# Kernel optimization log

Measured on AMD Instinct MI355X. Metric: run time of the kernel, lower is better.

Reference implementation:

```python
import jax, jax.numpy as jnp
import numpy as np

NEG_INF = -1.0e9  # masked_fill value in the original


def gaussian_prior(n_heads, len_q, len_k, dtype=jnp.float32):
    """Per-head lower-triangular Gaussian positional bias.

    gm[h, i, j] = exp(-(j - i)^2 / (2 * sigma_h^2)) for i >= j, else 0.
    The buggy source never passes sigma_hs; we use sigma_h = h + 1 as a
    deterministic per-head bandwidth (wider Gaussians for later heads).
    """
    i = jnp.arange(len_q)[:, None]          # [Lq, 1]
    j = jnp.arange(len_k)[None, :]          # [1, Lk]
    d2 = (j - i).astype(dtype) ** 2         # [Lq, Lk]
    sigma = jnp.arange(1, n_heads + 1, dtype=dtype)  # [H]
    g = jnp.exp(-d2[None] / (2.0 * sigma[:, None, None] ** 2))  # [H, Lq, Lk]
    return jnp.where(i >= j, g, jnp.zeros((), dtype))[None]     # mask upper tri -> [1,H,Lq,Lk] via broadcast of where


def setup_inputs() -> dict:
    key = jax.random.key(0)
    kq, kk, kv = jax.random.split(key, 3)
    B, H, S, D = 2, 16, 2048, 128
    Q = jax.random.normal(kq, (B, H, S, D), dtype=jnp.float32)
    K = jax.random.normal(kk, (B, H, S, D), dtype=jnp.float32)
    V = jax.random.normal(kv, (B, H, S, D), dtype=jnp.float32)
    # Causal mask: True where attention is disallowed (j > i), broadcastable.
    i = jnp.arange(S)[:, None]
    j = jnp.arange(S)[None, :]
    attn_mask = (j > i)[None, None]  # [1,1,S,S] bool
    return {"Q": Q, "K": K, "V": V, "attn_mask": attn_mask}


def reference(Q, K, V, attn_mask):
    B, H, Lq, D = Q.shape
    Lk = K.shape[2]
    scale = 1.0 / np.sqrt(D).astype(np.float32)
    # scores: [B,H,Lq,Lk]
    scores = jnp.einsum("bhqd,bhkd->bhqk", Q, K) * scale
    gm = gaussian_prior(H, Lq, Lk, dtype=scores.dtype)  # [H,Lq,Lk] broadcast over batch
    scores = scores + gm
    scores = jnp.where(attn_mask, jnp.asarray(NEG_INF, scores.dtype), scores)
    attn = jax.nn.softmax(scores, axis=-1)
    context = jnp.einsum("bhqk,bhkd->bhqd", attn, V)
    return (context, attn)
```

## Files before the change

### kernel.cpp

```cpp
#include <hip/hip_runtime.h>

typedef __attribute__((ext_vector_type(8))) short s16x8;
typedef __attribute__((ext_vector_type(4))) float f32x4;


static __device__ __forceinline__ unsigned short f2bf(float f) {
  unsigned int u = __float_as_uint(f);
  u += 0x7fffu + ((u >> 16) & 1u);
  return (unsigned short)(u >> 16);
}

static __device__ __forceinline__ unsigned short* swz(unsigned short* base, int row,
                                                      int shift, int byte_in_row) {
  int b = (row << shift) + (byte_in_row ^ ((row & 7) << 4));
  return (unsigned short*)((char*)base + b);
}

static __device__ __forceinline__ s16x8 pack8(float4 a, float4 b) {
  s16x8 p;
  p[0] = (short)f2bf(a.x); p[1] = (short)f2bf(a.y);
  p[2] = (short)f2bf(a.z); p[3] = (short)f2bf(a.w);
  p[4] = (short)f2bf(b.x); p[5] = (short)f2bf(b.y);
  p[6] = (short)f2bf(b.z); p[7] = (short)f2bf(b.w);
  return p;
}

#define GLDS(gp, lp) __builtin_amdgcn_global_load_lds(                        \
    (const __attribute__((address_space(1))) void*)(gp),                      \
    (__attribute__((address_space(3))) void*)(lp), 16, 0, 0)

#define STAGE(ldsbase, gtile) do {                                            \
    const char* _g = (const char*)(gtile) + (w << 12) + (lane << 4);          \
    char* _l = (char*)(ldsbase) + (w << 12);                                  \
    GLDS(_g,        _l);                                                      \
    GLDS(_g + 1024, _l + 1024);                                               \
    GLDS(_g + 2048, _l + 2048);                                               \
    GLDS(_g + 3072, _l + 3072);                                               \
  } while (0)

#define C_L2E   1.4426950408889634f
#define C_SCL2  (0.08838834764831845f * C_L2E)
#define C_B1    (-11.541560327111707f)


__global__ void pack_kv(const float* __restrict__ Kg, const float* __restrict__ Vg,
                        unsigned short* __restrict__ Kw, unsigned short* __restrict__ Vw) {
  __shared__ float Vs[8192];
  const int blk = (int)blockIdx.x;
  const float* Kb = Kg + ((size_t)blk << 13);
  const float* Vb = Vg + ((size_t)blk << 13);
  unsigned short* Ko = Kw + ((size_t)blk << 13);
  unsigned short* Vo = Vw + ((size_t)blk << 13);
  int c = (int)threadIdx.x;
  #pragma unroll
  for (int it = 0; it < 4; ++it, c += 256) {
    int r = c >> 4, c8 = (c & 15) << 3;
    int dst = r * 128 + ((((c8 << 1)) ^ ((r & 7) << 4)) >> 1);
    const float4* s4 = (const float4*)(Kb + r * 128 + c8);
    *(s16x8*)(Ko + dst) = pack8(s4[0], s4[1]);
  }
  c = (int)threadIdx.x;
  #pragma unroll
  for (int it = 0; it < 8; ++it, c += 256)
    *(float4*)(Vs + (c << 2)) = *(const float4*)(Vb + (c << 2));
  __syncthreads();
  c = (int)threadIdx.x;
  #pragma unroll
  for (int it = 0; it < 4; ++it, c += 256) {
    int d = c & 127, j0 = (c >> 7) << 3;
    s16x8 p;
    #pragma unroll
    for (int e = 0; e < 8; ++e) p[e] = (short)f2bf(Vs[(j0 + e) * 128 + d]);
    int dst = d * 64 + ((((j0 << 1)) ^ ((d & 7) << 4)) >> 1);
    *(s16x8*)(Vo + dst) = p;
  }
}


__global__ __launch_bounds__(256, 2)
void gpsdpa9(const float* __restrict__ Qg, const unsigned short* __restrict__ Kw,
             const unsigned short* __restrict__ Vw, float* __restrict__ Og,
             float* __restrict__ Ag) {
  __shared__ alignas(16) unsigned short KV[32768];
  __shared__ alignas(16) unsigned short Ps[4][1024];

  const int tid  = (int)threadIdx.x;
  const int w    = tid >> 6;
  const int lane = tid & 63;
  const int l15  = lane & 15;
  const int g    = lane >> 4;

  const int bh = (int)blockIdx.x & 31;
  const int qt = 31 - ((int)blockIdx.x >> 5);
  const int h  = bh & 15;
  const int q0 = qt << 6;

  const float* Qb = Qg + ((size_t)bh << 18) + ((size_t)q0 << 7);
  const unsigned short* Kb = Kw + ((size_t)(bh << 5) << 13);
  const unsigned short* Vb = Vw + ((size_t)(bh << 5) << 13);
  float* Ob = Og + ((size_t)bh << 18) + ((size_t)q0 << 7);
  float* Ab = Ag + ((size_t)bh << 22);

  const float cst2 = (-1.0f / (2.0f * (float)(h + 1) * (float)(h + 1))) * C_L2E;

  s16x8 aQ[4];
  {
    const float* qr = Qb + ((w << 4) + l15) * 128 + (g << 3);
    #pragma unroll
    for (int kc = 0; kc < 4; ++kc) {
      const float4* s4 = (const float4*)(qr + (kc << 5));
      aQ[kc] = pack8(s4[0], s4[1]);
    }
  }

  const int ibase = q0 + (w << 4) + (g << 2);
  const f32x4 fzero = {0.f, 0.f, 0.f, 0.f};

  float ps_acc[4] = {0.f, 0.f, 0.f, 0.f};

  const int nst = (qt >> 1) + 1;
  STAGE(&KV[0],    Kb);
  STAGE(&KV[8192], Kb + ((size_t)1 << 13));
  for (int s = 0; s < nst; ++s) {
    const int cur = s & 1;
    __syncthreads();
    if (s + 1 < nst) {
      unsigned short* nb = &KV[(cur ^ 1) << 14];
      STAGE(nb,        Kb + ((size_t)(2 * s + 2) << 13));
      STAGE(nb + 8192, Kb + ((size_t)(2 * s + 3) << 13));
    }
    #pragma unroll
    for (int half = 0; half < 2; ++half) {
      const int t = 2 * s + half;
      if (t > qt) break;
      unsigned short* Kt = &KV[(cur << 14) + (half << 13)];

      f32x4 acc[4];
      #pragma unroll
      for (int n = 0; n < 4; ++n) acc[n] = fzero;
      __builtin_amdgcn_s_setprio(1);
      #pragma unroll
      for (int kc = 0; kc < 4; ++kc) {
        #pragma unroll
        for (int n = 0; n < 4; ++n) {
          s16x8 bK = *(const s16x8*)swz(Kt, (n << 4) + l15, 8, (kc << 6) + (g << 4));
          acc[n] = __builtin_amdgcn_mfma_f32_16x16x32_bf16(aQ[kc], bK, acc[n], 0, 0, 0);
        }
      }
      __builtin_amdgcn_s_setprio(0);

      const int jb = (t << 6) + l15;
      if (t <= qt - 3) {
        #pragma unroll
        for (int r = 0; r < 4; ++r) {
          float sm = 0.f;
          #pragma unroll
          for (int n = 0; n < 4; ++n)
            sm += __builtin_amdgcn_exp2f(fmaf(acc[n][r], C_SCL2, C_B1));
          ps_acc[r] += sm;
        }
      } else if (t < qt) {
        #pragma unroll
        for (int r = 0; r < 4; ++r) {
          const int i = ibase + r;
          float sm = 0.f;
          #pragma unroll
          for (int n = 0; n < 4; ++n) {
            float fd = (float)(i - (jb + (n << 4)));
            float gl = __builtin_amdgcn_exp2f(fd * fd * cst2);
            sm += __builtin_amdgcn_exp2f(fmaf(acc[n][r], C_SCL2, fmaf(gl, C_L2E, C_B1)));
          }
          ps_acc[r] += sm;
        }
      } else {
        #pragma unroll
        for (int r = 0; r < 4; ++r) {
          const int i = ibase + r;
          float sm = 0.f;
          #pragma unroll
          for (int n = 0; n < 4; ++n) {
            int dist = i - (jb + (n << 4));
            float fd = (float)dist;
            float gl = __builtin_amdgcn_exp2f(fd * fd * cst2);
            float x = __builtin_amdgcn_exp2f(fmaf(acc[n][r], C_SCL2, fmaf(gl, C_L2E, C_B1)));
            sm += (dist >= 0) ? x : 0.f;
          }
          ps_acc[r] += sm;
        }
      }
    }
  }

  float lrs2[4];
  #pragma unroll
  for (int r = 0; r < 4; ++r) {
    float v = ps_acc[r];
    #pragma unroll
    for (int mk = 1; mk < 16; mk <<= 1) v += __shfl_xor(v, mk, 64);
    lrs2[r] = C_B1 - __log2f(v);
  }

  f32x4 oacc[8];
  #pragma unroll
  for (int dn = 0; dn < 8; ++dn) oacc[dn] = fzero;

  unsigned short* Pw = &Ps[w][0];

  __syncthreads();
  STAGE(&KV[0],     Kb);
  STAGE(&KV[16384], Vb);

  for (int t = 0; t <= qt; ++t) {
    const int cur = t & 1;
    __syncthreads();
    if (t < qt) {
      STAGE(&KV[(cur ^ 1) << 13],           Kb + ((size_t)(t + 1) << 13));
      STAGE(&KV[16384 + ((cur ^ 1) << 13)], Vb + ((size_t)(t + 1) << 13));
    }
    unsigned short* Kt = &KV[cur << 13];
    unsigned short* Vt = &KV[16384 + (cur << 13)];

    f32x4 acc[4];
    #pragma unroll
    for (int n = 0; n < 4; ++n) acc[n] = fzero;
    __builtin_amdgcn_s_setprio(1);
    #pragma unroll
    for (int kc = 0; kc < 4; ++kc) {
      #pragma unroll
      for (int n = 0; n < 4; ++n) {
        s16x8 bK = *(const s16x8*)swz(Kt, (n << 4) + l15, 8, (kc << 6) + (g << 4));
        acc[n] = __builtin_amdgcn_mfma_f32_16x16x32_bf16(aQ[kc], bK, acc[n], 0, 0, 0);
      }
    }
    __builtin_amdgcn_s_setprio(0);

    const int jb = (t << 6) + l15;
    if (t <= qt - 3) {
      #pragma unroll
      for (int r = 0; r < 4; ++r) {
        const int i = ibase + r;
        #pragma unroll
        for (int n = 0; n < 4; ++n) {
          float p = __builtin_amdgcn_exp2f(fmaf(acc[n][r], C_SCL2, lrs2[r]));
          Ab[(size_t)i * 2048 + jb + (n << 4)] = p;
          *swz(Pw, (g << 2) + r, 7, ((n << 4) + l15) << 1) = f2bf(p);
        }
      }
    } else if (t < qt) {
      #pragma unroll
      for (int r = 0; r < 4; ++r) {
        const int i = ibase + r;
        #pragma unroll
        for (int n = 0; n < 4; ++n) {
          float fd = (float)(i - (jb + (n << 4)));
          float gl = __builtin_amdgcn_exp2f(fd * fd * cst2);
          float p = __builtin_amdgcn_exp2f(fmaf(acc[n][r], C_SCL2, fmaf(gl, C_L2E, lrs2[r])));
          Ab[(size_t)i * 2048 + jb + (n << 4)] = p;
          *swz(Pw, (g << 2) + r, 7, ((n << 4) + l15) << 1) = f2bf(p);
        }
      }
    } else {
      #pragma unroll
      for (int r = 0; r < 4; ++r) {
        const int i = ibase + r;
        #pragma unroll
        for (int n = 0; n < 4; ++n) {
          int dist = i - (jb + (n << 4));
          float fd = (float)dist;
          float gl = __builtin_amdgcn_exp2f(fd * fd * cst2);
          float x = __builtin_amdgcn_exp2f(fmaf(acc[n][r], C_SCL2, fmaf(gl, C_L2E, lrs2[r])));
          float p = (dist >= 0) ? x : 0.f;
          Ab[(size_t)i * 2048 + jb + (n << 4)] = p;
          *swz(Pw, (g << 2) + r, 7, ((n << 4) + l15) << 1) = f2bf(p);
        }
      }
    }

    __builtin_amdgcn_s_setprio(1);
    #pragma unroll
    for (int kc2 = 0; kc2 < 2; ++kc2) {
      s16x8 pa = *(const s16x8*)swz(Pw, l15, 7, (kc2 << 6) + (g << 4));
      #pragma unroll
      for (int dn = 0; dn < 8; ++dn) {
        s16x8 vb = *(const s16x8*)swz(Vt, (dn << 4) + l15, 7, (kc2 << 6) + (g << 4));
        oacc[dn] = __builtin_amdgcn_mfma_f32_16x16x32_bf16(pa, vb, oacc[dn], 0, 0, 0);
      }
    }
    __builtin_amdgcn_s_setprio(0);
  }

  #pragma unroll
  for (int dn = 0; dn < 8; ++dn) {
    #pragma unroll
    for (int r = 0; r < 4; ++r) {
      Ob[(size_t)((w << 4) + (g << 2) + r) * 128 + (dn << 4) + l15] = oacc[dn][r];
    }
  }

  const float4 z4 = make_float4(0.f, 0.f, 0.f, 0.f);
  for (int tt = qt + 1; tt < 32; ++tt) {
    float4* dst = (float4*)(Ab + (size_t)q0 * 2048 + (tt << 6));
    int f = tid;
    #pragma unroll
    for (int k = 0; k < 4; ++k, f += 256) {
      int r = f >> 4, cc = f & 15;
      dst[(size_t)r * 512 + cc] = z4;
    }
  }
}


__global__ __launch_bounds__(256, 2)
void gpsdpa_fb(const float* __restrict__ Qg, const float* __restrict__ Kg,
               const float* __restrict__ Vg, float* __restrict__ Og,
               float* __restrict__ Ag) {
  __shared__ alignas(16) unsigned short Qs[64 * 128];
  __shared__ alignas(16) unsigned short Ksl[64 * 128];
  __shared__ alignas(16) unsigned short Vtl[128 * 64];
  __shared__ alignas(16) unsigned short Ps[4][16 * 64];
  __shared__ float gtab[2048];

  const int tid  = (int)threadIdx.x;
  const int w    = tid >> 6;
  const int lane = tid & 63;
  const int l15  = lane & 15;
  const int g    = lane >> 4;

  const int bh = (int)blockIdx.x & 31;
  const int qt = 31 - ((int)blockIdx.x >> 5);
  const int h  = bh & 15;
  const int q0 = qt << 6;

  const size_t base = (size_t)bh << 18;
  const float* Qb = Qg + base + (size_t)q0 * 128;
  const float* Kb = Kg + base;
  const float* Vb = Vg + base;
  float* Ob = Og + base;
  float* Ab = Ag + ((size_t)bh << 22);

  {
    float sig = (float)(h + 1);
    float c = -1.0f / (2.0f * sig * sig);
    for (int d = tid; d < 2048; d += 256) {
      float fd = (float)d;
      gtab[d] = __expf(fd * fd * c);
    }
  }

  {
    int c = tid;
    #pragma unroll
    for (int it = 0; it < 4; ++it, c += 256) {
      int r = c >> 4, c8 = (c & 15) << 3;
      const float4* s4 = (const float4*)(Qb + (size_t)r * 128 + c8);
      *(s16x8*)swz(Qs, r, 8, c8 * 2) = pack8(s4[0], s4[1]);
    }
  }
  __syncthreads();

  s16x8 aQ[4];
  #pragma unroll
  for (int kc = 0; kc < 4; ++kc)
    aQ[kc] = *(const s16x8*)swz(Qs, (w << 4) + l15, 8, (kc << 6) + (g << 4));

  const float scale = 0.08838834764831845f;
  const int ibase = q0 + (w << 4) + (g << 2);

  float m_r[4], ls_r[4];
  #pragma unroll
  for (int r = 0; r < 4; ++r) { m_r[r] = -3.0e38f; ls_r[r] = 0.0f; }

  const f32x4 fzero = {0.f, 0.f, 0.f, 0.f};

  for (int t = 0; t <= qt; ++t) {
    __syncthreads();
    {
      int c = tid;
      #pragma unroll
      for (int it = 0; it < 4; ++it, c += 256) {
        int r = c >> 4, c8 = (c & 15) << 3;
        const float4* s4 = (const float4*)(Kb + (size_t)((t << 6) + r) * 128 + c8);
        *(s16x8*)swz(Ksl, r, 8, c8 * 2) = pack8(s4[0], s4[1]);
      }
    }
    __syncthreads();

    f32x4 acc[4];
    #pragma unroll
    for (int n = 0; n < 4; ++n) acc[n] = fzero;
    #pragma unroll
    for (int kc = 0; kc < 4; ++kc) {
      #pragma unroll
      for (int n = 0; n < 4; ++n) {
        s16x8 bK = *(const s16x8*)swz(Ksl, (n << 4) + l15, 8, (kc << 6) + (g << 4));
        acc[n] = __builtin_amdgcn_mfma_f32_16x16x32_bf16(aQ[kc], bK, acc[n], 0, 0, 0);
      }
    }

    const int jb = (t << 6) + l15;
    #pragma unroll
    for (int r = 0; r < 4; ++r) {
      const int i = ibase + r;
      float sv[4];
      float mx = -3.0e38f;
      #pragma unroll
      for (int n = 0; n < 4; ++n) {
        int dist = i - (jb + (n << 4));
        float x = (dist >= 0) ? (acc[n][r] * scale + gtab[dist]) : -1.0e9f;
        sv[n] = x;
        mx = fmaxf(mx, x);
      }
      #pragma unroll
      for (int mk = 1; mk < 16; mk <<= 1) mx = fmaxf(mx, __shfl_xor(mx, mk, 64));
      float mn = fmaxf(m_r[r], mx);
      float sm = 0.f;
      #pragma unroll
      for (int n = 0; n < 4; ++n) sm += __expf(sv[n] - mn);
      #pragma unroll
      for (int mk = 1; mk < 16; mk <<= 1) sm += __shfl_xor(sm, mk, 64);
      ls_r[r] = ls_r[r] * __expf(m_r[r] - mn) + sm;
      m_r[r] = mn;
    }
  }

  float rls[4];
  #pragma unroll
  for (int r = 0; r < 4; ++r) rls[r] = 1.0f / ls_r[r];

  f32x4 oacc[8];
  #pragma unroll
  for (int dn = 0; dn < 8; ++dn) oacc[dn] = fzero;

  unsigned short* Pw = &Ps[w][0];

  for (int t = 0; t <= qt; ++t) {
    __syncthreads();
    {
      int c = tid;
      #pragma unroll
      for (int it = 0; it < 4; ++it, c += 256) {
        int r = c >> 4, c8 = (c & 15) << 3;
        const float4* s4 = (const float4*)(Kb + (size_t)((t << 6) + r) * 128 + c8);
        *(s16x8*)swz(Ksl, r, 8, c8 * 2) = pack8(s4[0], s4[1]);
      }
      c = tid;
      #pragma unroll
      for (int it = 0; it < 4; ++it, c += 256) {
        int d = c & 127, j0 = (c >> 7) << 3;
        const float* vs = Vb + (size_t)((t << 6) + j0) * 128 + d;
        s16x8 p;
        #pragma unroll
        for (int e = 0; e < 8; ++e) p[e] = (short)f2bf(vs[(size_t)e * 128]);
        *(s16x8*)swz(Vtl, d, 7, j0 * 2) = p;
      }
    }
    __syncthreads();

    f32x4 acc[4];
    #pragma unroll
    for (int n = 0; n < 4; ++n) acc[n] = fzero;
    #pragma unroll
    for (int kc = 0; kc < 4; ++kc) {
      #pragma unroll
      for (int n = 0; n < 4; ++n) {
        s16x8 bK = *(const s16x8*)swz(Ksl, (n << 4) + l15, 8, (kc << 6) + (g << 4));
        acc[n] = __builtin_amdgcn_mfma_f32_16x16x32_bf16(aQ[kc], bK, acc[n], 0, 0, 0);
      }
    }

    const int jb = (t << 6) + l15;
    #pragma unroll
    for (int r = 0; r < 4; ++r) {
      const int i = ibase + r;
      float* arow = Ab + (size_t)i * 2048 + (t << 6) + l15;
      #pragma unroll
      for (int n = 0; n < 4; ++n) {
        int dist = i - (jb + (n << 4));
        float x = (dist >= 0) ? (acc[n][r] * scale + gtab[dist]) : -1.0e9f;
        float p = __expf(x - m_r[r]) * rls[r];
        arow[n << 4] = p;
        *swz(Pw, (g << 2) + r, 7, ((n << 4) + l15) << 1) = f2bf(p);
      }
    }

    #pragma unroll
    for (int kc2 = 0; kc2 < 2; ++kc2) {
      s16x8 pa = *(const s16x8*)swz(Pw, l15, 7, (kc2 << 6) + (g << 4));
      #pragma unroll
      for (int dn = 0; dn < 8; ++dn) {
        s16x8 vb = *(const s16x8*)swz(Vtl, (dn << 4) + l15, 7, (kc2 << 6) + (g << 4));
        oacc[dn] = __builtin_amdgcn_mfma_f32_16x16x32_bf16(pa, vb, oacc[dn], 0, 0, 0);
      }
    }
  }

  #pragma unroll
  for (int dn = 0; dn < 8; ++dn) {
    #pragma unroll
    for (int r = 0; r < 4; ++r) {
      Ob[(size_t)(ibase + r) * 128 + (dn << 4) + l15] = oacc[dn][r];
    }
  }

  const int jmax = (qt + 1) << 6;
  if (jmax < 2048) {
    for (int r = 0; r < 64; ++r) {
      float4* dst = (float4*)(Ab + (size_t)(q0 + r) * 2048);
      for (int cv = (jmax >> 2) + tid; cv < 512; cv += 256) {
        dst[cv] = make_float4(0.f, 0.f, 0.f, 0.f);
      }
    }
  }
}


extern "C" void kernel_launch(void* const* d_in, const int* in_sizes, int n_in,
                              void* d_out, int out_size, void* d_ws, size_t ws_size,
                              hipStream_t stream) {
  (void)in_sizes; (void)n_in; (void)out_size;
  const float* Q = (const float*)d_in[0];
  const float* K = (const float*)d_in[1];
  const float* V = (const float*)d_in[2];
  float* ctx  = (float*)d_out;
  float* attn = ctx + (size_t)2 * 16 * 2048 * 128;

  const size_t NEED = (size_t)2 << 24;
  if (ws_size >= NEED) {
    unsigned short* Kw = (unsigned short*)d_ws;
    unsigned short* Vw = Kw + ((size_t)1 << 23);
    pack_kv<<<dim3(1024), dim3(256), 0, stream>>>(K, V, Kw, Vw);
    gpsdpa9<<<dim3(1024), dim3(256), 0, stream>>>(Q, Kw, Vw, ctx, attn);
  } else {
    gpsdpa_fb<<<dim3(1024), dim3(256), 0, stream>>>(Q, K, V, ctx, attn);
  }
}
```

Measured before the change: 208.2 us.

## Coalesce attention stores via LDS transpose and shrink LDS for more occupancy

The attention probabilities are staged as bf16 through a smaller per-warp LDS tile and then written back as row-contiguous float4 stores, replacing the scattered scalar fp32 stores. V goes from a double-buffered tile to a single buffer loaded each iteration, and the combined K/V buffer is split up. Together this cuts LDS use so launch bounds can ask for three blocks per CU instead of two. The trade-off is that the attention output now carries bf16 rounding instead of full fp32 values. It also adds an extra block barrier per iteration, and V loads now sit on the critical path with no prefetch.

```diff
diff --git a/kernel.cpp b/kernel.cpp
--- a/kernel.cpp
+++ b/kernel.cpp
@@ -10,9 +10,18 @@
   return (unsigned short)(u >> 16);
 }
 
+#define BLO(u) __uint_as_float((u) << 16)
+#define BHI(u) __uint_as_float((u) & 0xffff0000u)
+
 static __device__ __forceinline__ unsigned short* swz(unsigned short* base, int row,
                                                       int shift, int byte_in_row) {
   int b = (row << shift) + (byte_in_row ^ ((row & 7) << 4));
+  return (unsigned short*)((char*)base + b);
+}
+
+static __device__ __forceinline__ unsigned short* swzP(unsigned short* base, int row,
+                                                       int byte_in_row) {
+  int b = (row << 6) + (byte_in_row ^ ((row & 3) << 4));
   return (unsigned short*)((char*)base + b);
 }
 
@@ -77,12 +86,13 @@
 }
 
 
-__global__ __launch_bounds__(256, 2)
-void gpsdpa9(const float* __restrict__ Qg, const unsigned short* __restrict__ Kw,
-             const unsigned short* __restrict__ Vw, float* __restrict__ Og,
-             float* __restrict__ Ag) {
-  __shared__ alignas(16) unsigned short KV[32768];
-  __shared__ alignas(16) unsigned short Ps[4][1024];
+__global__ __launch_bounds__(256, 3)
+void gpsdpa10(const float* __restrict__ Qg, const unsigned short* __restrict__ Kw,
+              const unsigned short* __restrict__ Vw, float* __restrict__ Og,
+              float* __restrict__ Ag) {
+  __shared__ alignas(16) unsigned short Kbuf[2][8192];
+  __shared__ alignas(16) unsigned short Vbuf[8192];
+  __shared__ alignas(16) unsigned short Ps[4][512];
 
   const int tid  = (int)threadIdx.x;
   const int w    = tid >> 6;
@@ -118,107 +128,12 @@
 
   float ps_acc[4] = {0.f, 0.f, 0.f, 0.f};
 
-  const int nst = (qt >> 1) + 1;
-  STAGE(&KV[0],    Kb);
-  STAGE(&KV[8192], Kb + ((size_t)1 << 13));
-  for (int s = 0; s < nst; ++s) {
-    const int cur = s & 1;
-    __syncthreads();
-    if (s + 1 < nst) {
-      unsigned short* nb = &KV[(cur ^ 1) << 14];
-      STAGE(nb,        Kb + ((size_t)(2 * s + 2) << 13));
-      STAGE(nb + 8192, Kb + ((size_t)(2 * s + 3) << 13));
-    }
-    #pragma unroll
-    for (int half = 0; half < 2; ++half) {
-      const int t = 2 * s + half;
-      if (t > qt) break;
-      unsigned short* Kt = &KV[(cur << 14) + (half << 13)];
-
-      f32x4 acc[4];
-      #pragma unroll
-      for (int n = 0; n < 4; ++n) acc[n] = fzero;
-      __builtin_amdgcn_s_setprio(1);
-      #pragma unroll
-      for (int kc = 0; kc < 4; ++kc) {
-        #pragma unroll
-        for (int n = 0; n < 4; ++n) {
-          s16x8 bK = *(const s16x8*)swz(Kt, (n << 4) + l15, 8, (kc << 6) + (g << 4));
-          acc[n] = __builtin_amdgcn_mfma_f32_16x16x32_bf16(aQ[kc], bK, acc[n], 0, 0, 0);
-        }
-      }
-      __builtin_amdgcn_s_setprio(0);
-
-      const int jb = (t << 6) + l15;
-      if (t <= qt - 3) {
-        #pragma unroll
-        for (int r = 0; r < 4; ++r) {
-          float sm = 0.f;
-          #pragma unroll
-          for (int n = 0; n < 4; ++n)
-            sm += __builtin_amdgcn_exp2f(fmaf(acc[n][r], C_SCL2, C_B1));
-          ps_acc[r] += sm;
-        }
-      } else if (t < qt) {
-        #pragma unroll
-        for (int r = 0; r < 4; ++r) {
-          const int i = ibase + r;
-          float sm = 0.f;
-          #pragma unroll
-          for (int n = 0; n < 4; ++n) {
-            float fd = (float)(i - (jb + (n << 4)));
-            float gl = __builtin_amdgcn_exp2f(fd * fd * cst2);
-            sm += __builtin_amdgcn_exp2f(fmaf(acc[n][r], C_SCL2, fmaf(gl, C_L2E, C_B1)));
-          }
-          ps_acc[r] += sm;
-        }
-      } else {
-        #pragma unroll
-        for (int r = 0; r < 4; ++r) {
-          const int i = ibase + r;
-          float sm = 0.f;
-          #pragma unroll
-          for (int n = 0; n < 4; ++n) {
-            int dist = i - (jb + (n << 4));
-            float fd = (float)dist;
-            float gl = __builtin_amdgcn_exp2f(fd * fd * cst2);
-            float x = __builtin_amdgcn_exp2f(fmaf(acc[n][r], C_SCL2, fmaf(gl, C_L2E, C_B1)));
-            sm += (dist >= 0) ? x : 0.f;
-          }
-          ps_acc[r] += sm;
-        }
-      }
-    }
-  }
-
-  float lrs2[4];
-  #pragma unroll
-  for (int r = 0; r < 4; ++r) {
-    float v = ps_acc[r];
-    #pragma unroll
-    for (int mk = 1; mk < 16; mk <<= 1) v += __shfl_xor(v, mk, 64);
-    lrs2[r] = C_B1 - __log2f(v);
-  }
-
-  f32x4 oacc[8];
-  #pragma unroll
-  for (int dn = 0; dn < 8; ++dn) oacc[dn] = fzero;
-
-  unsigned short* Pw = &Ps[w][0];
-
-  __syncthreads();
-  STAGE(&KV[0],     Kb);
-  STAGE(&KV[16384], Vb);
-
+  STAGE(&Kbuf[0][0], Kb);
   for (int t = 0; t <= qt; ++t) {
     const int cur = t & 1;
     __syncthreads();
-    if (t < qt) {
-      STAGE(&KV[(cur ^ 1) << 13],           Kb + ((size_t)(t + 1) << 13));
-      STAGE(&KV[16384 + ((cur ^ 1) << 13)], Vb + ((size_t)(t + 1) << 13));
-    }
-    unsigned short* Kt = &KV[cur << 13];
-    unsigned short* Vt = &KV[16384 + (cur << 13)];
+    if (t < qt) STAGE(&Kbuf[cur ^ 1][0], Kb + ((size_t)(t + 1) << 13));
+    unsigned short* Kt = &Kbuf[cur][0];
 
     f32x4 acc[4];
     #pragma unroll
@@ -238,25 +153,102 @@
     if (t <= qt - 3) {
       #pragma unroll
       for (int r = 0; r < 4; ++r) {
-        const int i = ibase + r;
-        #pragma unroll
-        for (int n = 0; n < 4; ++n) {
-          float p = __builtin_amdgcn_exp2f(fmaf(acc[n][r], C_SCL2, lrs2[r]));
-          Ab[(size_t)i * 2048 + jb + (n << 4)] = p;
-          *swz(Pw, (g << 2) + r, 7, ((n << 4) + l15) << 1) = f2bf(p);
-        }
+        float sm = 0.f;
+        #pragma unroll
+        for (int n = 0; n < 4; ++n)
+          sm += __builtin_amdgcn_exp2f(fmaf(acc[n][r], C_SCL2, C_B1));
+        ps_acc[r] += sm;
       }
     } else if (t < qt) {
       #pragma unroll
       for (int r = 0; r < 4; ++r) {
         const int i = ibase + r;
+        float sm = 0.f;
         #pragma unroll
         for (int n = 0; n < 4; ++n) {
           float fd = (float)(i - (jb + (n << 4)));
           float gl = __builtin_amdgcn_exp2f(fd * fd * cst2);
-          float p = __builtin_amdgcn_exp2f(fmaf(acc[n][r], C_SCL2, fmaf(gl, C_L2E, lrs2[r])));
-          Ab[(size_t)i * 2048 + jb + (n << 4)] = p;
-          *swz(Pw, (g << 2) + r, 7, ((n << 4) + l15) << 1) = f2bf(p);
+          sm += __builtin_amdgcn_exp2f(fmaf(acc[n][r], C_SCL2, fmaf(gl, C_L2E, C_B1)));
+        }
+        ps_acc[r] += sm;
+      }
+    } else {
+      #pragma unroll
+      for (int r = 0; r < 4; ++r) {
+        const int i = ibase + r;
+        float sm = 0.f;
+        #pragma unroll
+        for (int n = 0; n < 4; ++n) {
+          int dist = i - (jb + (n << 4));
+          float fd = (float)dist;
+          float gl = __builtin_amdgcn_exp2f(fd * fd * cst2);
+          float x = __builtin_amdgcn_exp2f(fmaf(acc[n][r], C_SCL2, fmaf(gl, C_L2E, C_B1)));
+          sm += (dist >= 0) ? x : 0.f;
+        }
+        ps_acc[r] += sm;
+      }
+    }
+  }
+
+  float lrs2[4];
+  #pragma unroll
+  for (int r = 0; r < 4; ++r) {
+    float v = ps_acc[r];
+    #pragma unroll
+    for (int mk = 1; mk < 16; mk <<= 1) v += __shfl_xor(v, mk, 64);
+    lrs2[r] = C_B1 - __log2f(v);
+  }
+
+  f32x4 oacc[8];
+  #pragma unroll
+  for (int dn = 0; dn < 8; ++dn) oacc[dn] = fzero;
+
+  unsigned short* Pw = &Ps[w][0];
+
+  __syncthreads();
+  STAGE(&Kbuf[0][0], Kb);
+  asm volatile("s_waitcnt vmcnt(0)" ::: "memory");
+
+  for (int t = 0; t <= qt; ++t) {
+    const int cur = t & 1;
+    __builtin_amdgcn_s_barrier();
+    __builtin_amdgcn_sched_barrier(0);
+    if (t < qt) STAGE(&Kbuf[cur ^ 1][0], Kb + ((size_t)(t + 1) << 13));
+    STAGE(&Vbuf[0], Vb + ((size_t)t << 13));
+
+    unsigned short* Kt = &Kbuf[cur][0];
+
+    f32x4 acc[4];
+    #pragma unroll
+    for (int n = 0; n < 4; ++n) acc[n] = fzero;
+    __builtin_amdgcn_s_setprio(1);
+    #pragma unroll
+    for (int kc = 0; kc < 4; ++kc) {
+      #pragma unroll
+      for (int n = 0; n < 4; ++n) {
+        s16x8 bK = *(const s16x8*)swz(Kt, (n << 4) + l15, 8, (kc << 6) + (g << 4));
+        acc[n] = __builtin_amdgcn_mfma_f32_16x16x32_bf16(aQ[kc], bK, acc[n], 0, 0, 0);
+      }
+    }
+    __builtin_amdgcn_s_setprio(0);
+
+    float p[4][4];
+    const int jb = (t << 6) + l15;
+    if (t <= qt - 3) {
+      #pragma unroll
+      for (int r = 0; r < 4; ++r)
+        #pragma unroll
+        for (int n = 0; n < 4; ++n)
+          p[r][n] = __builtin_amdgcn_exp2f(fmaf(acc[n][r], C_SCL2, lrs2[r]));
+    } else if (t < qt) {
+      #pragma unroll
+      for (int r = 0; r < 4; ++r) {
+        const int i = ibase + r;
+        #pragma unroll
+        for (int n = 0; n < 4; ++n) {
+          float fd = (float)(i - (jb + (n << 4)));
+          float gl = __builtin_amdgcn_exp2f(fd * fd * cst2);
+          p[r][n] = __builtin_amdgcn_exp2f(fmaf(acc[n][r], C_SCL2, fmaf(gl, C_L2E, lrs2[r])));
         }
       }
     } else {
@@ -269,24 +261,46 @@
           float fd = (float)dist;
           float gl = __builtin_amdgcn_exp2f(fd * fd * cst2);
           float x = __builtin_amdgcn_exp2f(fmaf(acc[n][r], C_SCL2, fmaf(gl, C_L2E, lrs2[r])));
-          float p = (dist >= 0) ? x : 0.f;
-          Ab[(size_t)i * 2048 + jb + (n << 4)] = p;
-          *swz(Pw, (g << 2) + r, 7, ((n << 4) + l15) << 1) = f2bf(p);
+          p[r][n] = (dist >= 0) ? x : 0.f;
         }
       }
     }
 
+    s16x8 pa[2];
+    uint4 ua[2];
+    #pragma unroll
+    for (int hh = 0; hh < 2; ++hh) {
+      #pragma unroll
+      for (int r = 0; r < 4; ++r) {
+        #pragma unroll
+        for (int nn = 0; nn < 2; ++nn)
+          *swzP(Pw, (g << 2) + r, ((nn << 4) + l15) << 1) = f2bf(p[r][(hh << 1) + nn]);
+      }
+      pa[hh] = *(const s16x8*)swzP(Pw, l15, g << 4);
+      ua[hh] = *(const uint4*)swzP(Pw, lane >> 2, (lane & 3) << 4);
+    }
+
+    __syncthreads();
     __builtin_amdgcn_s_setprio(1);
     #pragma unroll
     for (int kc2 = 0; kc2 < 2; ++kc2) {
-      s16x8 pa = *(const s16x8*)swz(Pw, l15, 7, (kc2 << 6) + (g << 4));
       #pragma unroll
       for (int dn = 0; dn < 8; ++dn) {
-        s16x8 vb = *(const s16x8*)swz(Vt, (dn << 4) + l15, 7, (kc2 << 6) + (g << 4));
-        oacc[dn] = __builtin_amdgcn_mfma_f32_16x16x32_bf16(pa, vb, oacc[dn], 0, 0, 0);
+        int vrow = (dn << 4) + l15;
+        s16x8 vb = *(const s16x8*)swz(&Vbuf[0], vrow, 7, (kc2 << 6) + (g << 4));
+        oacc[dn] = __builtin_amdgcn_mfma_f32_16x16x32_bf16(pa[kc2], vb, oacc[dn], 0, 0, 0);
       }
     }
     __builtin_amdgcn_s_setprio(0);
+
+    {
+      const int row = lane >> 2, c0 = (lane & 3) << 3;
+      float* arow = Ab + (size_t)(q0 + (w << 4) + row) * 2048 + (t << 6) + c0;
+      *(float4*)(arow)      = make_float4(BLO(ua[0].x), BHI(ua[0].x), BLO(ua[0].y), BHI(ua[0].y));
+      *(float4*)(arow + 4)  = make_float4(BLO(ua[0].z), BHI(ua[0].z), BLO(ua[0].w), BHI(ua[0].w));
+      *(float4*)(arow + 32) = make_float4(BLO(ua[1].x), BHI(ua[1].x), BLO(ua[1].y), BHI(ua[1].y));
+      *(float4*)(arow + 36) = make_float4(BLO(ua[1].z), BHI(ua[1].z), BLO(ua[1].w), BHI(ua[1].w));
+    }
   }
 
   #pragma unroll
@@ -529,7 +543,7 @@
     unsigned short* Kw = (unsigned short*)d_ws;
     unsigned short* Vw = Kw + ((size_t)1 << 23);
     pack_kv<<<dim3(1024), dim3(256), 0, stream>>>(K, V, Kw, Vw);
-    gpsdpa9<<<dim3(1024), dim3(256), 0, stream>>>(Q, Kw, Vw, ctx, attn);
+    gpsdpa10<<<dim3(1024), dim3(256), 0, stream>>>(Q, Kw, Vw, ctx, attn);
   } else {
     gpsdpa_fb<<<dim3(1024), dim3(256), 0, stream>>>(Q, K, V, ctx, attn);
   }
```

Result: slower. 220.5 us (+5.9%).
